# Performance work log

Measured on AMD Instinct MI355X. Metric: run time of the kernel, lower is better.

Reference implementation:

```python
import jax, jax.numpy as jnp
import numpy as np

DIM = 768
NUM_HEADS = 12
HEAD_DIM = DIM // NUM_HEADS
SCALE = HEAD_DIM ** -0.5


def setup_inputs() -> dict:
    key = jax.random.key(0)
    ks = jax.random.split(key, 8)
    B, Nx, Ny = 4, 1024, 2048
    std = DIM ** -0.5
    return {
        "x": jax.random.normal(ks[0], (B, Nx, DIM), dtype=jnp.float32),
        "y": jax.random.normal(ks[1], (B, Ny, DIM), dtype=jnp.float32),
        "Wq": jax.random.normal(ks[2], (DIM, DIM), dtype=jnp.float32) * std,
        "Wk": jax.random.normal(ks[3], (DIM, DIM), dtype=jnp.float32) * std,
        "Wv": jax.random.normal(ks[4], (DIM, DIM), dtype=jnp.float32) * std,
        "Wproj": jax.random.normal(ks[5], (DIM, DIM), dtype=jnp.float32) * std,
        "bproj": jnp.zeros((DIM,), dtype=jnp.float32),
    }


def reference(x, y, Wq, Wk, Wv, Wproj, bproj):
    B, Nx, C = x.shape
    Ny = y.shape[1]
    H, D = NUM_HEADS, HEAD_DIM
    # Linear projections (torch nn.Linear: x @ W.T), then split heads -> [B,H,N,D]
    q = (x @ Wq.T).reshape(B, Nx, H, D).transpose(0, 2, 1, 3)
    k = (y @ Wk.T).reshape(B, Ny, H, D).transpose(0, 2, 1, 3)
    v = (y @ Wv.T).reshape(B, Ny, H, D).transpose(0, 2, 1, 3)
    # Manual attention: full [B,H,Nx,Ny] score matrix (faithful to source)
    attn = jnp.einsum("bhqd,bhkd->bhqk", q, k) * SCALE
    attn = jax.nn.softmax(attn, axis=-1)
    out = jnp.einsum("bhqk,bhkd->bhqd", attn, v)
    out = out.transpose(0, 2, 1, 3).reshape(B, Nx, C)
    return out @ Wproj.T + bproj
```

## Files before the change

kernel.cpp:

```cpp
#include <hip/hip_runtime.h>
#include <hip/hip_bf16.h>

typedef unsigned short u16;
typedef __attribute__((ext_vector_type(8))) short bf16x8;
typedef __attribute__((ext_vector_type(4))) float f32x4;
typedef __attribute__((ext_vector_type(16))) float f32x16;
typedef __attribute__((ext_vector_type(4))) unsigned u32x4;

#define MFMA(a, b, c) __builtin_amdgcn_mfma_f32_16x16x32_bf16(a, b, c, 0, 0, 0)
#define MFMA32(a, b, c) __builtin_amdgcn_mfma_f32_32x32x16_bf16(a, b, c, 0, 0, 0)

#define STAGE16(g, l) __builtin_amdgcn_global_load_lds( \
    (const __attribute__((address_space(1))) void*)(g),  \
    (__attribute__((address_space(3))) void*)(l), 16, 0, 0)

#define EXP2(x) __builtin_amdgcn_exp2f(x)

__device__ __forceinline__ u16 f2bf(float f) {
  union { float f; unsigned u; } v; v.f = f;
  return (u16)((v.u + 0x7fffu + ((v.u >> 16) & 1u)) >> 16);
}

__device__ __forceinline__ unsigned pack_bf2(float lo, float hi) {
  unsigned r;
  asm("v_cvt_pk_bf16_f32 %0, %1, %2" : "=v"(r) : "v"(lo), "v"(hi));
  return r;
}

__device__ __forceinline__ void pl32swap(unsigned &a, unsigned &b) {
  asm("v_permlane32_swap_b32 %0, %1" : "+v"(a), "+v"(b));
}

__global__ __launch_bounds__(256) void convert_all(
    const float* __restrict__ x, const float* __restrict__ y,
    const float* __restrict__ wq, const float* __restrict__ wk,
    const float* __restrict__ wv, const float* __restrict__ wp,
    u16* __restrict__ xb, u16* __restrict__ yb,
    u16* __restrict__ wqb, u16* __restrict__ wkb,
    u16* __restrict__ wvb, u16* __restrict__ wpb)
{
  constexpr int G0 = 4096 * 768 / 4;
  constexpr int G1 = G0 + 8192 * 768 / 4;
  constexpr int GW = 768 * 768 / 4;
  int g = blockIdx.x * 256 + threadIdx.x;
  const float* s; u16* d; int o;
  if      (g < G0)          { s = x;  d = xb;  o = g; }
  else if (g < G1)          { s = y;  d = yb;  o = g - G0; }
  else if (g < G1 + GW)     { s = wq; d = wqb; o = g - G1; }
  else if (g < G1 + 2*GW)   { s = wk; d = wkb; o = g - G1 - GW; }
  else if (g < G1 + 3*GW)   { s = wv; d = wvb; o = g - G1 - 2*GW; }
  else if (g < G1 + 4*GW)   { s = wp; d = wpb; o = g - G1 - 3*GW; }
  else return;
  float4 v = reinterpret_cast<const float4*>(s)[o];
  ushort4 r;
  r.x = f2bf(v.x); r.y = f2bf(v.y); r.z = f2bf(v.z); r.w = f2bf(v.w);
  reinterpret_cast<ushort4*>(d)[o] = r;
}

template <bool PROJ>
__global__ __launch_bounds__(256) void gemm_k(
    const u16* __restrict__ A0, const u16* __restrict__ A1,
    const u16* __restrict__ W0, const u16* __restrict__ W1,
    const u16* __restrict__ W2,
    u16* __restrict__ Qa, u16* __restrict__ Ka, u16* __restrict__ Vw,
    const float* __restrict__ bias, float* __restrict__ fout)
{
  __shared__ u16 sA[2][128 * 64];
  __shared__ u16 sB[2][128 * 64];

  const int nper = PROJ ? 24 : 120;
  int bid = (blockIdx.x & 7) * nper + (blockIdx.x >> 3);

  const u16 *A, *W;
  int mode, mt, nt;
  if (PROJ)           { mode = 3; A = A0; W = W0; mt = bid / 6;        nt = bid % 6; }
  else if (bid < 192) { mode = 0; A = A0; W = W0; mt = bid / 6;        nt = bid % 6; }
  else if (bid < 576) { mode = 1; A = A1; W = W1; mt = (bid-192) / 6;  nt = (bid-192) % 6; }
  else                { mode = 2; A = A1; W = W2; mt = (bid-576) / 6;  nt = (bid-576) % 6; }

  const int tid = threadIdx.x;
  const int w = tid >> 6, l = tid & 63;
  const int wm = w >> 1, wn = w & 1;
  const int g = l >> 4, m = l & 15;

  const int mbase = mt * 128, nbase = nt * 128;

  const int srow = l >> 3;
  const int schunk = ((l & 7) ^ srow) * 8;
  const u16* Ag = A + (size_t)(mbase + srow) * 768 + schunk;
  const u16* Wg = W + (size_t)(nbase + srow) * 768 + schunk;

  f32x4 acc[4][4] = {};

#pragma unroll
  for (int i = 0; i < 4; ++i) {
    const int ri = (i * 4 + w) * 8;
    STAGE16(Ag + (size_t)ri * 768, (char*)sA[0] + ri * 128);
    STAGE16(Wg + (size_t)ri * 768, (char*)sB[0] + ri * 128);
  }

  for (int kt = 0; kt < 12; ++kt) {
    __syncthreads();

    if (kt < 11) {
      const int ko = (kt + 1) * 64;
      const int nb = (kt + 1) & 1;
#pragma unroll
      for (int i = 0; i < 4; ++i) {
        const int ri = (i * 4 + w) * 8;
        STAGE16(Ag + (size_t)ri * 768 + ko, (char*)sA[nb] + ri * 128);
        STAGE16(Wg + (size_t)ri * 768 + ko, (char*)sB[nb] + ri * 128);
      }
    }

    const int cb = kt & 1;
    bf16x8 af[2][4], bfr[2][4];
#pragma unroll
    for (int c = 0; c < 2; ++c)
#pragma unroll
      for (int t = 0; t < 4; ++t) {
        const int ar = wm * 64 + t * 16 + m;
        const int br = wn * 64 + t * 16 + m;
        const int cp = ((c * 4 + g) ^ (l & 7)) * 16;
        af[c][t]  = *reinterpret_cast<const bf16x8*>((const char*)sA[cb] + ar * 128 + cp);
        bfr[c][t] = *reinterpret_cast<const bf16x8*>((const char*)sB[cb] + br * 128 + cp);
      }
#pragma unroll
    for (int c = 0; c < 2; ++c)
#pragma unroll
      for (int mi = 0; mi < 4; ++mi)
#pragma unroll
        for (int ni = 0; ni < 4; ++ni)
          acc[mi][ni] = MFMA(af[c][mi], bfr[c][ni], acc[mi][ni]);
  }

  const float QSCALE = 0.18033688011112042f;
  const int rowb = mbase + wm * 64 + g * 4;
  const int colb = nbase + wn * 64 + m;
#pragma unroll
  for (int mi = 0; mi < 4; ++mi) {
#pragma unroll
    for (int ni = 0; ni < 4; ++ni) {
      const int col = colb + ni * 16;
      const int h = col >> 6, d = col & 63;
      const int t_ = d >> 4, hh = (d >> 3) & 1, di = d & 7;
      const int fo = t_ * 512 + hh * 256 + di;
      if constexpr (PROJ) {
#pragma unroll
        for (int r = 0; r < 4; ++r) {
          const int row = rowb + mi * 16 + r;
          fout[(size_t)row * 768 + col] = acc[mi][ni][r] + bias[col];
        }
      } else {
        if (mode == 0) {
#pragma unroll
          for (int r = 0; r < 4; ++r) {
            const int row = rowb + mi * 16 + r;
            const int b_ = row >> 10, n = row & 1023;
            Qa[((size_t)(b_ * 12 + h) * 32 + (n >> 5)) * 2048 + fo + (n & 31) * 8] =
                f2bf(acc[mi][ni][r] * QSCALE);
          }
        } else if (mode == 1) {
#pragma unroll
          for (int r = 0; r < 4; ++r) {
            const int row = rowb + mi * 16 + r;
            const int b_ = row >> 11, n = row & 2047;
            Ka[(size_t)(b_ * 12 + h) * 131072 + (n >> 5) * 2048 + fo + (n & 31) * 8] =
                f2bf(acc[mi][ni][r]);
          }
        } else {
          const int row = rowb + mi * 16;
          const int b_ = row >> 11, n = row & 2047;
          ushort4 pk;
          pk.x = f2bf(acc[mi][ni][0]); pk.y = f2bf(acc[mi][ni][1]);
          pk.z = f2bf(acc[mi][ni][2]); pk.w = f2bf(acc[mi][ni][3]);
          *reinterpret_cast<ushort4*>(
              Vw + (size_t)(b_ * 12 + h) * 131072 + (n >> 3) * 512 + d * 8 + (n & 7)) = pk;
        }
      }
    }
  }
}

__global__ __launch_bounds__(256, 4) void attn_fwd(
    const u16* __restrict__ Qa, const u16* __restrict__ Ka,
    const u16* __restrict__ Vw, u16* __restrict__ AOb)
{
  __shared__ u16 sK[2][4096];
  __shared__ u16 sV[2][4096];

  const int bid = blockIdx.x;
  const int bh = bid % 48, qt = bid / 48;
  const int tid = threadIdx.x;
  const int w = tid >> 6, l = tid & 63;
  const int h = l >> 5, q = l & 31;

  const u16* qb = Qa + (size_t)(bh * 32 + qt * 4 + w) * 2048 + h * 256 + q * 8;
  bf16x8 qf[4];
#pragma unroll
  for (int t = 0; t < 4; ++t)
    qf[t] = *reinterpret_cast<const bf16x8*>(qb + t * 512);

  const u16* Kbh = Ka + (size_t)bh * 131072;
  const u16* Vbh = Vw + (size_t)bh * 131072;

  const int sbase = w * 1024;
  const u16* Ksrc = Kbh + sbase + l * 8;
  const u16* Vsrc = Vbh + sbase + l * 8;

  f32x16 o0 = {}, o1 = {};
  float lrun = 0.f;

#pragma unroll
  for (int i = 0; i < 2; ++i) {
    STAGE16(Ksrc + i * 512, (char*)&sK[0][sbase + i * 512]);
    STAGE16(Vsrc + i * 512, (char*)&sV[0][sbase + i * 512]);
  }

  for (int kt = 0; kt < 32; ++kt) {
    __syncthreads();

    if (kt < 31) {
      const int nb = (kt + 1) & 1;
      const size_t go = (size_t)(kt + 1) * 4096;
#pragma unroll
      for (int i = 0; i < 2; ++i) {
        STAGE16(Ksrc + go + i * 512, (char*)&sK[nb][sbase + i * 512]);
        STAGE16(Vsrc + go + i * 512, (char*)&sV[nb][sbase + i * 512]);
      }
    }

    const u16* kp = &sK[kt & 1][0];
    const u16* vp = &sV[kt & 1][0];

    bf16x8 kf0[4], kf1[4];
#pragma unroll
    for (int t = 0; t < 4; ++t) {
      kf0[t] = *reinterpret_cast<const bf16x8*>(kp + t * 512 + h * 256 + q * 8);
      kf1[t] = *reinterpret_cast<const bf16x8*>(kp + 2048 + t * 512 + h * 256 + q * 8);
    }

    f32x16 s0 = {}, s1 = {};
    __builtin_amdgcn_s_setprio(1);
#pragma unroll
    for (int t = 0; t < 4; ++t) {
      s0 = MFMA32(kf0[t], qf[t], s0);
      s1 = MFMA32(kf1[t], qf[t], s1);
    }
    __builtin_amdgcn_s_setprio(0);

    bf16x8 vf0[4], vf1[4];
#pragma unroll
    for (int t = 0; t < 4; ++t) {
      vf0[t] = *reinterpret_cast<const bf16x8*>(vp + t * 1024 + h * 512 + q * 8);
      vf1[t] = *reinterpret_cast<const bf16x8*>(vp + t * 1024 + h * 512 + q * 8 + 256);
    }

    float p0[16], p1[16];
#pragma unroll
    for (int r = 0; r < 16; ++r) p0[r] = EXP2(s0[r]);
#pragma unroll
    for (int r = 0; r < 16; ++r) p1[r] = EXP2(s1[r]);

    float a8[8];
#pragma unroll
    for (int i = 0; i < 8; ++i)
      a8[i] = (p0[2*i] + p0[2*i+1]) + (p1[2*i] + p1[2*i+1]);
    lrun += ((a8[0]+a8[1]) + (a8[2]+a8[3])) + ((a8[4]+a8[5]) + (a8[6]+a8[7]));

    unsigned pk[2][4][2];
#pragma unroll
    for (int qd = 0; qd < 4; ++qd) {
      pk[0][qd][0] = pack_bf2(p0[4*qd+0], p0[4*qd+1]);
      pk[0][qd][1] = pack_bf2(p0[4*qd+2], p0[4*qd+3]);
      pk[1][qd][0] = pack_bf2(p1[4*qd+0], p1[4*qd+1]);
      pk[1][qd][1] = pack_bf2(p1[4*qd+2], p1[4*qd+3]);
    }

    __builtin_amdgcn_s_setprio(1);
#pragma unroll
    for (int t = 0; t < 4; ++t) {
      const int c = t >> 1, j0 = 2 * (t & 1);
      unsigned x0 = pk[c][j0][0], y0 = pk[c][j0 + 1][0];
      unsigned x1 = pk[c][j0][1], y1 = pk[c][j0 + 1][1];
      pl32swap(x0, y0);
      pl32swap(x1, y1);
      u32x4 fv; fv[0] = x0; fv[1] = x1; fv[2] = y0; fv[3] = y1;
      const bf16x8 af = __builtin_bit_cast(bf16x8, fv);
      o0 = MFMA32(af, vf0[t], o0);
      o1 = MFMA32(af, vf1[t], o1);
    }
    __builtin_amdgcn_s_setprio(0);
  }

  lrun += __shfl_xor(lrun, 32);
  const int b_ = bh / 12, hd = bh % 12;
  const int q0 = (qt * 4 + w) * 32;
#pragma unroll
  for (int r = 0; r < 16; ++r) {
    const int crow = (r >> 2) * 8 + 4 * h + (r & 3);
    const float rl = 1.f / __shfl(lrun, crow);
    u16* dst = AOb + ((size_t)b_ * 1024 + q0 + crow) * 768 + hd * 64 + q;
    dst[0]  = f2bf(o0[r] * rl);
    dst[32] = f2bf(o1[r] * rl);
  }
}

extern "C" void kernel_launch(void* const* d_in, const int* in_sizes, int n_in,
                              void* d_out, int out_size, void* d_ws, size_t ws_size,
                              hipStream_t stream)
{
  const float* x  = (const float*)d_in[0];
  const float* y  = (const float*)d_in[1];
  const float* wq = (const float*)d_in[2];
  const float* wk = (const float*)d_in[3];
  const float* wv = (const float*)d_in[4];
  const float* wp = (const float*)d_in[5];
  const float* bp = (const float*)d_in[6];
  float* out = (float*)d_out;

  char* ws = (char*)d_ws;
  u16* xb  = (u16*)ws; ws += (size_t)4096 * 768 * 2;
  u16* yb  = (u16*)ws; ws += (size_t)8192 * 768 * 2;
  u16* wqb = (u16*)ws; ws += (size_t)768 * 768 * 2;
  u16* wkb = (u16*)ws; ws += (size_t)768 * 768 * 2;
  u16* wvb = (u16*)ws; ws += (size_t)768 * 768 * 2;
  u16* wpb = (u16*)ws; ws += (size_t)768 * 768 * 2;
  u16* Qa  = (u16*)ws; ws += (size_t)4096 * 768 * 2;
  u16* Ka  = (u16*)ws; ws += (size_t)8192 * 768 * 2;
  u16* Vw  = (u16*)ws; ws += (size_t)8192 * 768 * 2;
  u16* AOb = (u16*)ws; ws += (size_t)4096 * 768 * 2;

  convert_all<<<11520, 256, 0, stream>>>(x, y, wq, wk, wv, wp,
                                         xb, yb, wqb, wkb, wvb, wpb);
  gemm_k<false><<<960, 256, 0, stream>>>(xb, yb, wqb, wkb, wvb,
                                         Qa, Ka, Vw, nullptr, nullptr);
  attn_fwd<<<384, 256, 0, stream>>>(Qa, Ka, Vw, AOb);
  gemm_k<true><<<192, 256, 0, stream>>>(AOb, nullptr, wpb, nullptr, nullptr,
                                        nullptr, nullptr, nullptr, bp, out);
}
```

Baseline: 120.1 us.

## Split attention over two KV halves and merge partials in a combine kernel

The attention kernel now splits each head's 2048 keys into two halves, doubling the grid from 384 to 768 blocks so the work spreads more evenly across CUs. Each block writes its unnormalized fp32 partial output and row sums to workspace. A new combine kernel adds the two partials, normalizes them, converts to bf16 and writes the head-interleaved layout the projection GEMM expects. The cost is an extra launch plus roughly 25MB of fp32 partials written and read back. The merge is only correct if both halves use the same softmax offset, since no max rescaling is done.

```diff
diff --git a/kernel.cpp b/kernel.cpp
--- a/kernel.cpp
+++ b/kernel.cpp
@@ -184,25 +184,28 @@
 
 __global__ __launch_bounds__(256, 4) void attn_fwd(
     const u16* __restrict__ Qa, const u16* __restrict__ Ka,
-    const u16* __restrict__ Vw, u16* __restrict__ AOb)
+    const u16* __restrict__ Vw, float* __restrict__ Opart,
+    float* __restrict__ Lpart)
 {
   __shared__ u16 sK[2][4096];
   __shared__ u16 sV[2][4096];
 
   const int bid = blockIdx.x;
-  const int bh = bid % 48, qt = bid / 48;
+  const int bh = bid % 48;
+  const int rest = bid / 48;
+  const int qb = rest & 7, half = rest >> 3;
   const int tid = threadIdx.x;
   const int w = tid >> 6, l = tid & 63;
   const int h = l >> 5, q = l & 31;
 
-  const u16* qb = Qa + (size_t)(bh * 32 + qt * 4 + w) * 2048 + h * 256 + q * 8;
+  const u16* qbp = Qa + (size_t)(bh * 32 + qb * 4 + w) * 2048 + h * 256 + q * 8;
   bf16x8 qf[4];
 #pragma unroll
   for (int t = 0; t < 4; ++t)
-    qf[t] = *reinterpret_cast<const bf16x8*>(qb + t * 512);
-
-  const u16* Kbh = Ka + (size_t)bh * 131072;
-  const u16* Vbh = Vw + (size_t)bh * 131072;
+    qf[t] = *reinterpret_cast<const bf16x8*>(qbp + t * 512);
+
+  const u16* Kbh = Ka + (size_t)bh * 131072 + (size_t)half * 65536;
+  const u16* Vbh = Vw + (size_t)bh * 131072 + (size_t)half * 65536;
 
   const int sbase = w * 1024;
   const u16* Ksrc = Kbh + sbase + l * 8;
@@ -217,10 +220,10 @@
     STAGE16(Vsrc + i * 512, (char*)&sV[0][sbase + i * 512]);
   }
 
-  for (int kt = 0; kt < 32; ++kt) {
+  for (int kt = 0; kt < 16; ++kt) {
     __syncthreads();
 
-    if (kt < 31) {
+    if (kt < 15) {
       const int nb = (kt + 1) & 1;
       const size_t go = (size_t)(kt + 1) * 4096;
 #pragma unroll
@@ -294,16 +297,37 @@
   }
 
   lrun += __shfl_xor(lrun, 32);
-  const int b_ = bh / 12, hd = bh % 12;
-  const int q0 = (qt * 4 + w) * 32;
+  const int q0b = qb * 128 + w * 32;
+  float* Op = Opart + ((size_t)(half * 48 + bh) * 1024 + q0b) * 64;
 #pragma unroll
   for (int r = 0; r < 16; ++r) {
     const int crow = (r >> 2) * 8 + 4 * h + (r & 3);
-    const float rl = 1.f / __shfl(lrun, crow);
-    u16* dst = AOb + ((size_t)b_ * 1024 + q0 + crow) * 768 + hd * 64 + q;
-    dst[0]  = f2bf(o0[r] * rl);
-    dst[32] = f2bf(o1[r] * rl);
-  }
+    Op[crow * 64 + q]      = o0[r];
+    Op[crow * 64 + 32 + q] = o1[r];
+  }
+  if (l < 32)
+    Lpart[(size_t)(half * 48 + bh) * 1024 + q0b + l] = lrun;
+}
+
+__global__ __launch_bounds__(256) void combine(
+    const float* __restrict__ Opart, const float* __restrict__ Lpart,
+    u16* __restrict__ AOb)
+{
+  const int id = blockIdx.x * 256 + threadIdx.x;
+  const int d4 = id & 15;
+  const int bn = id >> 4;
+  const float4* O0 = reinterpret_cast<const float4*>(Opart);
+  const float4 a = O0[(size_t)bn * 16 + d4];
+  const float4 b = O0[(size_t)(49152 + bn) * 16 + d4];
+  const float rl = 1.f / (Lpart[bn] + Lpart[49152 + bn]);
+  ushort4 r;
+  r.x = f2bf((a.x + b.x) * rl);
+  r.y = f2bf((a.y + b.y) * rl);
+  r.z = f2bf((a.z + b.z) * rl);
+  r.w = f2bf((a.w + b.w) * rl);
+  const int bh = bn >> 10, n = bn & 1023;
+  *reinterpret_cast<ushort4*>(
+      AOb + ((size_t)(bh / 12) * 1024 + n) * 768 + (bh % 12) * 64 + d4 * 4) = r;
 }
 
 extern "C" void kernel_launch(void* const* d_in, const int* in_sizes, int n_in,
@@ -330,12 +354,15 @@
   u16* Ka  = (u16*)ws; ws += (size_t)8192 * 768 * 2;
   u16* Vw  = (u16*)ws; ws += (size_t)8192 * 768 * 2;
   u16* AOb = (u16*)ws; ws += (size_t)4096 * 768 * 2;
+  float* Opart = (float*)ws; ws += (size_t)2 * 48 * 1024 * 64 * 4;
+  float* Lpart = (float*)ws; ws += (size_t)2 * 48 * 1024 * 4;
 
   convert_all<<<11520, 256, 0, stream>>>(x, y, wq, wk, wv, wp,
                                          xb, yb, wqb, wkb, wvb, wpb);
   gemm_k<false><<<960, 256, 0, stream>>>(xb, yb, wqb, wkb, wvb,
                                          Qa, Ka, Vw, nullptr, nullptr);
-  attn_fwd<<<384, 256, 0, stream>>>(Qa, Ka, Vw, AOb);
+  attn_fwd<<<768, 256, 0, stream>>>(Qa, Ka, Vw, Opart, Lpart);
+  combine<<<3072, 256, 0, stream>>>(Opart, Lpart, AOb);
   gemm_k<true><<<192, 256, 0, stream>>>(AOb, nullptr, wpb, nullptr, nullptr,
                                         nullptr, nullptr, nullptr, bp, out);
 }
```

After: 114.1 us. -5.0%, faster.
